# Performance work log

Hardware: AMD Instinct MI355X
Metric: run time of the kernel (lower is better)

Reference implementation:

```python
import jax, jax.numpy as jnp
import numpy as np

E, H_HEADS, WS = 512, 16, 8
HEAD_D = E // H_HEADS
LN_EPS = 1e-5


def layernorm(x, g, b):
    mu = jnp.mean(x, axis=-1, keepdims=True)
    var = jnp.mean((x - mu) ** 2, axis=-1, keepdims=True)
    return (x - mu) / jnp.sqrt(var + LN_EPS) * g + b


def setup_inputs() -> dict:
    key = jax.random.key(0)
    ks = jax.random.split(key, 10)
    s = 0.02
    return {
        "x": jax.random.normal(ks[0], (4, 4096, E), jnp.float32),
        "in_proj_w": jax.random.normal(ks[1], (3 * E, E), jnp.float32) * s,
        "in_proj_b": jnp.zeros((3 * E,), jnp.float32),
        "out_w": jax.random.normal(ks[2], (E, E), jnp.float32) * s,
        "out_b": jnp.zeros((E,), jnp.float32),
        "ln1_g": jnp.ones((E,), jnp.float32),
        "ln1_b": jnp.zeros((E,), jnp.float32),
        "w1": jax.random.normal(ks[3], (4 * E, E), jnp.float32) * s,
        "b1": jnp.zeros((4 * E,), jnp.float32),
        "w2": jax.random.normal(ks[4], (E, 4 * E), jnp.float32) * s,
        "b2": jnp.zeros((E,), jnp.float32),
        "ln2_g": jnp.ones((E,), jnp.float32),
        "ln2_b": jnp.zeros((E,), jnp.float32),
        "num_patches_h": 64,
        "num_patches_w": 64,
    }


def reference(x, in_proj_w, in_proj_b, out_w, out_b, ln1_g, ln1_b,
              w1, b1, w2, b2, ln2_g, ln2_b, num_patches_h, num_patches_w):
    B, P, _ = x.shape
    Hp, Wp = num_patches_h, num_patches_w  # 64 divisible by WS -> no padding branch
    nwh, nww = Hp // WS, Wp // WS
    # window partition: (B, Hp, Wp, E) -> (B*nW, WS*WS, E)
    xw = x.reshape(B, nwh, WS, nww, WS, E).transpose(0, 1, 3, 2, 4, 5)
    xw = xw.reshape(B * nwh * nww, WS * WS, E)
    # nn.MultiheadAttention default batch_first=False: axis0 is SEQ (L=B*nW),
    # axis1 is BATCH (N=WS*WS). Reproduce that literal semantics.
    L, N = xw.shape[0], xw.shape[1]
    qkv = xw @ in_proj_w.T + in_proj_b          # (L, N, 3E)
    q, k, v = jnp.split(qkv, 3, axis=-1)
    qh = q.reshape(L, N, H_HEADS, HEAD_D)
    kh = k.reshape(L, N, H_HEADS, HEAD_D)
    vh = v.reshape(L, N, H_HEADS, HEAD_D)
    scale = 1.0 / np.sqrt(HEAD_D)
    scores = jnp.einsum('lnhd,mnhd->nhlm', qh, kh) * scale  # (N, h, L, L)
    attn = jax.nn.softmax(scores, axis=-1)
    o = jnp.einsum('nhlm,mnhd->lnhd', attn, vh).reshape(L, N, E)
    attn_out = o @ out_w.T + out_b
    y = layernorm(xw + attn_out, ln1_g, ln1_b)
    ffn = jax.nn.gelu(y @ w1.T + b1, approximate=False) @ w2.T + b2
    y = layernorm(y + ffn, ln2_g, ln2_b)
    # window unpartition
    y = y.reshape(B, nwh, nww, WS, WS, E).transpose(0, 1, 3, 2, 4, 5)
    return y.reshape(B, Hp * Wp, E)[:, :P, :]
```

## Files before the change

### kernel.cpp

```cpp
#include <hip/hip_runtime.h>
#include <cmath>


typedef _Float16 half8 __attribute__((ext_vector_type(8)));
typedef _Float16 half4v __attribute__((ext_vector_type(4)));
typedef float f32x4 __attribute__((ext_vector_type(4)));

#define GLOBAL_AS(p) ((const __attribute__((address_space(1))) void*)(p))
#define LDS_AS(p) ((__attribute__((address_space(3))) void*)(p))

__device__ __forceinline__ void gload_lds16(const _Float16* g, _Float16* l) {
  __builtin_amdgcn_global_load_lds(GLOBAL_AS(g), LDS_AS(l), 16, 0, 0);
}

__device__ __forceinline__ float wave_sum(float v) {
#pragma unroll
  for (int off = 32; off > 0; off >>= 1) v += __shfl_xor(v, off, 64);
  return v;
}

__device__ __forceinline__ float gelu_fast(float x) {
  const float y = 1.5957691216057308f * (x + 0.044715f * x * x * x);
  const float e = __expf(y);
  const float t = 1.0f - 2.0f / (e + 1.0f);
  return 0.5f * x * (1.0f + t);
}

__global__ __launch_bounds__(256) void castw4_kernel(
    const float* __restrict__ s0, _Float16* __restrict__ d0,
    const float* __restrict__ s1, _Float16* __restrict__ d1,
    const float* __restrict__ s2, _Float16* __restrict__ d2,
    const float* __restrict__ s3, _Float16* __restrict__ d3) {
  int b = blockIdx.x;
  const float* s; _Float16* d;
  if (b < 768) { s = s0; d = d0; }
  else if (b < 1024) { s = s1; d = d1; b -= 768; }
  else if (b < 2048) { s = s2; d = d2; b -= 1024; }
  else { s = s3; d = d3; b -= 2048; }
  const int i = (b * 256 + threadIdx.x) * 4;
  const float4 v = *(const float4*)&s[i];
  half4v o;
  o[0] = (_Float16)v.x; o[1] = (_Float16)v.y; o[2] = (_Float16)v.z; o[3] = (_Float16)v.w;
  *(half4v*)&d[i] = o;
}

__global__ __launch_bounds__(256) void gather_x_kernel(const float* __restrict__ x,
                                                       _Float16* __restrict__ xw) {
  const int idx = blockIdx.x * 256 + threadIdx.x;
  const int t = idx >> 6;
  const int e0 = (idx & 63) << 3;
  const int l = t >> 6, n = t & 63;
  const int bb = l >> 6, wh = (l >> 3) & 7, ww = l & 7;
  const int pi = n >> 3, pj = n & 7;
  const int xrow = (bb * 4096 + (wh * 8 + pi) * 64 + (ww * 8 + pj)) * 512;
  const float4 a = *(const float4*)&x[xrow + e0];
  const float4 b = *(const float4*)&x[xrow + e0 + 4];
  half8 o;
  o[0] = (_Float16)a.x; o[1] = (_Float16)a.y; o[2] = (_Float16)a.z; o[3] = (_Float16)a.w;
  o[4] = (_Float16)b.x; o[5] = (_Float16)b.y; o[6] = (_Float16)b.z; o[7] = (_Float16)b.w;
  *(half8*)&xw[t * 512 + e0] = o;
}

template <int EPI, int K>
__global__ __launch_bounds__(512, 2) void gemm8_kernel(
    const _Float16* __restrict__ A, const _Float16* __restrict__ B,
    const float* __restrict__ bias, _Float16* __restrict__ C, int N) {
  constexpr int NT = K / 64;
  constexpr int TA = 256 * 64;
  constexpr int TB = 128 * 64;
  constexpr int TT = TA + TB;
  __shared__ _Float16 L[3][TT];

  const int tid = threadIdx.x, lane = tid & 63, wave = tid >> 6;
  const int wr = wave >> 1, wc = wave & 1;
  const int lr = lane & 15, g = lane >> 4;

  const int nbn = N >> 7;
  const int cpx = gridDim.x >> 3;
  const int wg = (blockIdx.x & 7) * cpx + (blockIdx.x >> 3);
  const int bm = wg / nbn, bn = wg % nbn;

  const int scol = ((lane & 7) ^ (lane >> 3)) << 3;
  const int srow = lane >> 3;
  const _Float16* aS = A + (size_t)(bm * 256 + wave * 8 + srow) * K + scol;
  const _Float16* bS = B + (size_t)(bn * 128 + wave * 8 + srow) * K + scol;

  auto stage = [&](int s, int tt, int h) {
    const int koff = tt * 64;
    _Float16* Ls = &L[s][0];
    if (h == 0) {
      gload_lds16(aS + (size_t)0 * 64 * K + koff, &Ls[(0 * 64 + wave * 8) * 64]);
      gload_lds16(aS + (size_t)1 * 64 * K + koff, &Ls[(1 * 64 + wave * 8) * 64]);
      gload_lds16(aS + (size_t)2 * 64 * K + koff, &Ls[(2 * 64 + wave * 8) * 64]);
    } else {
      gload_lds16(aS + (size_t)3 * 64 * K + koff, &Ls[(3 * 64 + wave * 8) * 64]);
      gload_lds16(bS + (size_t)0 * 64 * K + koff, &Ls[TA + (0 * 64 + wave * 8) * 64]);
      gload_lds16(bS + (size_t)1 * 64 * K + koff, &Ls[TA + (1 * 64 + wave * 8) * 64]);
    }
  };

  const int sw0 = ((g ^ (lr & 7)) << 3);
  const int sw1 = (((4 + g) ^ (lr & 7)) << 3);
  int arow[4], brow[4];
#pragma unroll
  for (int m = 0; m < 4; ++m) arow[m] = (wr * 64 + m * 16 + lr) * 64;
#pragma unroll
  for (int n = 0; n < 4; ++n) brow[n] = TA + (wc * 64 + n * 16 + lr) * 64;

  f32x4 acc[4][4] = {};

  stage(0, 0, 0); stage(0, 0, 1);
  stage(1, 1, 0); stage(1, 1, 1);
  asm volatile("s_waitcnt vmcnt(6)" ::: "memory");
  asm volatile("s_barrier" ::: "memory");

  int p = 0, s = 2;
  for (int t = 0; t < NT; ++t) {
    const _Float16* Lp = &L[p][0];
    half8 af[4], bf[4];
#pragma unroll
    for (int m = 0; m < 4; ++m) af[m] = *(const half8*)&Lp[arow[m] + sw0];
#pragma unroll
    for (int n = 0; n < 4; ++n) bf[n] = *(const half8*)&Lp[brow[n] + sw0];
    if (t + 2 < NT) stage(s, t + 2, 0);
    __builtin_amdgcn_s_setprio(1);
#pragma unroll
    for (int m = 0; m < 4; ++m)
#pragma unroll
      for (int n = 0; n < 4; ++n)
        acc[m][n] = __builtin_amdgcn_mfma_f32_16x16x32_f16(af[m], bf[n], acc[m][n], 0, 0, 0);
    __builtin_amdgcn_s_setprio(0);
#pragma unroll
    for (int m = 0; m < 4; ++m) af[m] = *(const half8*)&Lp[arow[m] + sw1];
#pragma unroll
    for (int n = 0; n < 4; ++n) bf[n] = *(const half8*)&Lp[brow[n] + sw1];
    if (t + 2 < NT) stage(s, t + 2, 1);
    __builtin_amdgcn_s_setprio(1);
#pragma unroll
    for (int m = 0; m < 4; ++m)
#pragma unroll
      for (int n = 0; n < 4; ++n)
        acc[m][n] = __builtin_amdgcn_mfma_f32_16x16x32_f16(af[m], bf[n], acc[m][n], 0, 0, 0);
    __builtin_amdgcn_s_setprio(0);
    asm volatile("s_waitcnt lgkmcnt(0)" ::: "memory");
    if (t + 2 < NT)      asm volatile("s_waitcnt vmcnt(6)" ::: "memory");
    else if (t + 1 < NT) asm volatile("s_waitcnt vmcnt(0)" ::: "memory");
    asm volatile("s_barrier" ::: "memory");
    p = (p == 2) ? 0 : p + 1;
    s = (s == 2) ? 0 : s + 1;
  }

  float bsv[4];
#pragma unroll
  for (int n = 0; n < 4; ++n) bsv[n] = bias[bn * 128 + wc * 64 + n * 16 + lr];
  _Float16* Lc = &L[0][0] + wave * 4096;
#pragma unroll
  for (int m = 0; m < 4; ++m)
#pragma unroll
    for (int n = 0; n < 4; ++n)
#pragma unroll
      for (int r = 0; r < 4; ++r) {
        float v = acc[m][n][r] + bsv[n];
        if (EPI == 1) v = gelu_fast(v);
        const int row = m * 16 + g * 4 + r;
        const int col = n * 16 + lr;
        Lc[row * 64 + (col ^ ((row & 7) << 3))] = (_Float16)v;
      }
  asm volatile("s_waitcnt lgkmcnt(0)" ::: "memory");
  const int rrow = lane >> 3, slot = lane & 7;
  const int grow = bm * 256 + wr * 64;
  const int gcol = bn * 128 + wc * 64 + slot * 8;
#pragma unroll
  for (int blk = 0; blk < 8; ++blk) {
    const int row = blk * 8 + rrow;
    const half8 vv = *(const half8*)&Lc[row * 64 + ((slot ^ (row & 7)) << 3)];
    *(half8*)&C[(size_t)(grow + row) * N + gcol] = vv;
  }
}

__global__ __launch_bounds__(256) void attn_kernel(const _Float16* __restrict__ qkv,
                                                   _Float16* __restrict__ o_out) {
  const int n = blockIdx.x & 63;
  const int h = blockIdx.x >> 6;
  __shared__ _Float16 Ksh[256 * 40];
  __shared__ _Float16 Vt[32 * 264];
  __shared__ _Float16 Pw[4 * 64 * 72];
  const int tid = threadIdx.x;
  const int wq = tid >> 6, lane = tid & 63;
  const int lr = lane & 15, g = lane >> 4;
  const int hq = h * 32;

#pragma unroll
  for (int pass = 0; pass < 4; ++pass) {
    const int e = pass * 2048 + tid * 8;
    const int m = e >> 5, d = e & 31;
    const int base = (m * 64 + n) * 1536 + hq;
    const half8 k8 = *(const half8*)&qkv[base + 512 + d];
    const half8 v8 = *(const half8*)&qkv[base + 1024 + d];
    *(half8*)&Ksh[m * 40 + d] = k8;
#pragma unroll
    for (int j = 0; j < 8; ++j) Vt[(d + j) * 264 + m] = v8[j];
  }
  half8 qf[4];
#pragma unroll
  for (int qt = 0; qt < 4; ++qt) {
    const int qg = wq * 64 + qt * 16 + lr;
    qf[qt] = *(const half8*)&qkv[(qg * 64 + n) * 1536 + hq + g * 8];
  }
  __syncthreads();

  f32x4 o[4][2] = {};
  float den[4] = {0.f, 0.f, 0.f, 0.f};
  const float scale = 0.17677669529663687f;
  _Float16* P = &Pw[wq * (64 * 72)];

  for (int it = 0; it < 4; ++it) {
    const int k0 = it * 64;
#pragma unroll
    for (int qt = 0; qt < 4; ++qt) {
#pragma unroll
      for (int kt = 0; kt < 4; ++kt) {
        const half8 kf = *(const half8*)&Ksh[(k0 + kt * 16 + lr) * 40 + g * 8];
        const f32x4 z = {0.f, 0.f, 0.f, 0.f};
        f32x4 st = __builtin_amdgcn_mfma_f32_16x16x32_f16(kf, qf[qt], z, 0, 0, 0);
        const float p0 = __expf(st[0] * scale);
        const float p1 = __expf(st[1] * scale);
        const float p2 = __expf(st[2] * scale);
        const float p3 = __expf(st[3] * scale);
        den[qt] += (p0 + p1) + (p2 + p3);
        half4v w;
        w[0] = (_Float16)p0; w[1] = (_Float16)p1;
        w[2] = (_Float16)p2; w[3] = (_Float16)p3;
        *(half4v*)&P[(qt * 16 + lr) * 72 + kt * 16 + g * 4] = w;
      }
    }
    __syncthreads();
#pragma unroll
    for (int qt = 0; qt < 4; ++qt) {
#pragma unroll
      for (int ks = 0; ks < 2; ++ks) {
        const half8 pf = *(const half8*)&P[(qt * 16 + lr) * 72 + ks * 32 + g * 8];
#pragma unroll
        for (int dt = 0; dt < 2; ++dt) {
          const half8 vf = *(const half8*)&Vt[(dt * 16 + lr) * 264 + k0 + ks * 32 + g * 8];
          o[qt][dt] = __builtin_amdgcn_mfma_f32_16x16x32_f16(pf, vf, o[qt][dt], 0, 0, 0);
        }
      }
    }
    __syncthreads();
  }

#pragma unroll
  for (int qt = 0; qt < 4; ++qt) {
    float dq = den[qt];
    dq += __shfl_xor(dq, 16);
    dq += __shfl_xor(dq, 32);
    const float inv = 1.0f / dq;
#pragma unroll
    for (int r = 0; r < 4; ++r) {
      const float invr = __shfl(inv, g * 4 + r);
      const int qg = wq * 64 + qt * 16 + g * 4 + r;
      const int obase = (qg * 64 + n) * 512 + hq;
#pragma unroll
      for (int dt = 0; dt < 2; ++dt)
        o_out[obase + dt * 16 + lr] = (_Float16)(o[qt][dt][r] * invr);
    }
  }
}

template <int FINAL>
__global__ __launch_bounds__(256) void ln_kernel(
    const float* __restrict__ res32, const _Float16* __restrict__ add16,
    const float* __restrict__ g, const float* __restrict__ b,
    float* __restrict__ out32, _Float16* __restrict__ out16) {
  const int t = blockIdx.x * 4 + (threadIdx.x >> 6);
  const int lane = threadIdx.x & 63;
  const int e0 = lane << 3;
  const int l = t >> 6, n = t & 63;
  const int bb = l >> 6, wh = (l >> 3) & 7, ww = l & 7;
  const int pi = n >> 3, pj = n & 7;
  const int xrow = (bb * 4096 + (wh * 8 + pi) * 64 + (ww * 8 + pj)) * 512;
  const int trow = t * 512;
  const int rbase = (FINAL ? trow : xrow) + e0;
  const float4 ra = *(const float4*)&res32[rbase];
  const float4 rb = *(const float4*)&res32[rbase + 4];
  const half8 a8 = *(const half8*)&add16[trow + e0];
  float v[8];
  v[0] = ra.x + (float)a8[0]; v[1] = ra.y + (float)a8[1];
  v[2] = ra.z + (float)a8[2]; v[3] = ra.w + (float)a8[3];
  v[4] = rb.x + (float)a8[4]; v[5] = rb.y + (float)a8[5];
  v[6] = rb.z + (float)a8[6]; v[7] = rb.w + (float)a8[7];
  float sm = 0.f;
#pragma unroll
  for (int e = 0; e < 8; ++e) sm += v[e];
  sm = wave_sum(sm);
  const float mu = sm * (1.0f / 512.0f);
  float vs = 0.f;
#pragma unroll
  for (int e = 0; e < 8; ++e) { const float d = v[e] - mu; vs += d * d; }
  vs = wave_sum(vs);
  const float rstd = rsqrtf(vs * (1.0f / 512.0f) + 1e-5f);
  const float4 g1 = *(const float4*)&g[e0];
  const float4 g2 = *(const float4*)&g[e0 + 4];
  const float4 b1 = *(const float4*)&b[e0];
  const float4 b2 = *(const float4*)&b[e0 + 4];
  float y[8];
  y[0] = (v[0] - mu) * rstd * g1.x + b1.x; y[1] = (v[1] - mu) * rstd * g1.y + b1.y;
  y[2] = (v[2] - mu) * rstd * g1.z + b1.z; y[3] = (v[3] - mu) * rstd * g1.w + b1.w;
  y[4] = (v[4] - mu) * rstd * g2.x + b2.x; y[5] = (v[5] - mu) * rstd * g2.y + b2.y;
  y[6] = (v[6] - mu) * rstd * g2.z + b2.z; y[7] = (v[7] - mu) * rstd * g2.w + b2.w;
  if (FINAL) {
    *(float4*)&out32[xrow + e0] = make_float4(y[0], y[1], y[2], y[3]);
    *(float4*)&out32[xrow + e0 + 4] = make_float4(y[4], y[5], y[6], y[7]);
  } else {
    *(float4*)&out32[trow + e0] = make_float4(y[0], y[1], y[2], y[3]);
    *(float4*)&out32[trow + e0 + 4] = make_float4(y[4], y[5], y[6], y[7]);
    half8 o16;
#pragma unroll
    for (int e = 0; e < 8; ++e) o16[e] = (_Float16)y[e];
    *(half8*)&out16[trow + e0] = o16;
  }
}

extern "C" void kernel_launch(void* const* d_in, const int* in_sizes, int n_in,
                              void* d_out, int out_size, void* d_ws, size_t ws_size,
                              hipStream_t stream) {
  const float* x    = (const float*)d_in[0];
  const float* ipw  = (const float*)d_in[1];
  const float* ipb  = (const float*)d_in[2];
  const float* outw = (const float*)d_in[3];
  const float* outb = (const float*)d_in[4];
  const float* ln1g = (const float*)d_in[5];
  const float* ln1b = (const float*)d_in[6];
  const float* w1   = (const float*)d_in[7];
  const float* b1   = (const float*)d_in[8];
  const float* w2   = (const float*)d_in[9];
  const float* b2   = (const float*)d_in[10];
  const float* ln2g = (const float*)d_in[11];
  const float* ln2b = (const float*)d_in[12];
  float* out = (float*)d_out;
  char* ws = (char*)d_ws;

  _Float16* wqkv_h = (_Float16*)(ws + 0);
  _Float16* wout_h = (_Float16*)(ws + 1572864);
  _Float16* w1_h   = (_Float16*)(ws + 2097152);
  _Float16* w2_h   = (_Float16*)(ws + 4194304);
  _Float16* xw_h   = (_Float16*)(ws + 6291456);
  _Float16* qkv_h  = (_Float16*)(ws + 23068672);
  _Float16* attn_h = (_Float16*)(ws + 90177536);
  _Float16* ao_h   = (_Float16*)(ws + 106954752);
  float*    y32    = (float*)(ws + 123731968);
  _Float16* h_h = qkv_h;
  _Float16* f_h = attn_h;
  _Float16* y16 = xw_h;

  castw4_kernel<<<3072, 256, 0, stream>>>(ipw, wqkv_h, outw, wout_h, w1, w1_h, w2, w2_h);
  gather_x_kernel<<<4096, 256, 0, stream>>>(x, xw_h);
  gemm8_kernel<0, 512><<<768, 512, 0, stream>>>(xw_h, wqkv_h, ipb, qkv_h, 1536);
  attn_kernel<<<1024, 256, 0, stream>>>(qkv_h, attn_h);
  gemm8_kernel<0, 512><<<256, 512, 0, stream>>>(attn_h, wout_h, outb, ao_h, 512);
  ln_kernel<0><<<4096, 256, 0, stream>>>(x, ao_h, ln1g, ln1b, y32, y16);
  gemm8_kernel<1, 512><<<1024, 512, 0, stream>>>(y16, w1_h, b1, h_h, 2048);
  gemm8_kernel<0, 2048><<<256, 512, 0, stream>>>(h_h, w2_h, b2, f_h, 512);
  ln_kernel<1><<<4096, 256, 0, stream>>>(y32, f_h, ln2g, ln2b, out, nullptr);
}
```

Baseline: 225.6 us.

## Add 256x256-tile GEMM kernel for QKV and FFN1 projections

Adds a new GEMM variant with a 256x256 output tile per workgroup, double-buffered LDS instead of triple-buffered, and 8 waves arranged 2x4 with each wave computing 128x64. It replaces the 256x128 kernel for the QKV projection and the first FFN GEMM. The larger tile raises arithmetic intensity and reuse of A and B tiles, which cuts global and LDS traffic per FLOP. In exchange each wave holds 128 accumulator values, which raises register pressure and may lower occupancy. The grids are also halved, so there are fewer workgroups to spread across the CUs.

New measurement: 251.0 us. 1.11x slower.

```diff
diff --git a/kernel.cpp b/kernel.cpp
--- a/kernel.cpp
+++ b/kernel.cpp
@@ -59,6 +59,111 @@
   o[0] = (_Float16)a.x; o[1] = (_Float16)a.y; o[2] = (_Float16)a.z; o[3] = (_Float16)a.w;
   o[4] = (_Float16)b.x; o[5] = (_Float16)b.y; o[6] = (_Float16)b.z; o[7] = (_Float16)b.w;
   *(half8*)&xw[t * 512 + e0] = o;
+}
+
+template <int EPI, int K>
+__global__ __launch_bounds__(512, 2) void gemm16_kernel(
+    const _Float16* __restrict__ A, const _Float16* __restrict__ B,
+    const float* __restrict__ bias, _Float16* __restrict__ C, int N) {
+  constexpr int NT = K / 64;
+  constexpr int TA = 256 * 64;
+  constexpr int TT = 2 * TA;
+  __shared__ _Float16 L[2][TT];
+
+  const int tid = threadIdx.x, lane = tid & 63, wave = tid >> 6;
+  const int wr = wave >> 2, wc = wave & 3;
+  const int lr = lane & 15, g = lane >> 4;
+
+  const int nbn = N >> 8;
+  const int cpx = gridDim.x >> 3;
+  const int wg = (blockIdx.x & 7) * cpx + (blockIdx.x >> 3);
+  const int bm = wg / nbn, bn = wg % nbn;
+
+  const int scol = ((lane & 7) ^ (lane >> 3)) << 3;
+  const int srow = lane >> 3;
+  const _Float16* aS = A + (size_t)(bm * 256 + wave * 8 + srow) * K + scol;
+  const _Float16* bS = B + (size_t)(bn * 256 + wave * 8 + srow) * K + scol;
+
+  auto stage = [&](int b, int tt) {
+    const int koff = tt * 64;
+    _Float16* Ls = &L[b][0];
+#pragma unroll
+    for (int i = 0; i < 4; ++i)
+      gload_lds16(aS + (size_t)(i * 64) * K + koff, &Ls[(i * 64 + wave * 8) * 64]);
+#pragma unroll
+    for (int i = 0; i < 4; ++i)
+      gload_lds16(bS + (size_t)(i * 64) * K + koff, &Ls[TA + (i * 64 + wave * 8) * 64]);
+  };
+
+  const int sw0 = ((g ^ (lr & 7)) << 3);
+  const int sw1 = (((4 + g) ^ (lr & 7)) << 3);
+  int arow[8], brow[4];
+#pragma unroll
+  for (int m = 0; m < 8; ++m) arow[m] = (wr * 128 + m * 16 + lr) * 64;
+#pragma unroll
+  for (int n = 0; n < 4; ++n) brow[n] = TA + (wc * 64 + n * 16 + lr) * 64;
+
+  f32x4 acc[8][4] = {};
+
+  stage(0, 0);
+  __syncthreads();
+
+  for (int t = 0; t < NT; ++t) {
+    const int p = t & 1;
+    const _Float16* Lp = &L[p][0];
+    if (t + 1 < NT) stage(p ^ 1, t + 1);
+    half8 af[8], bf[4];
+#pragma unroll
+    for (int m = 0; m < 8; ++m) af[m] = *(const half8*)&Lp[arow[m] + sw0];
+#pragma unroll
+    for (int n = 0; n < 4; ++n) bf[n] = *(const half8*)&Lp[brow[n] + sw0];
+    __builtin_amdgcn_s_setprio(1);
+#pragma unroll
+    for (int m = 0; m < 8; ++m)
+#pragma unroll
+      for (int n = 0; n < 4; ++n)
+        acc[m][n] = __builtin_amdgcn_mfma_f32_16x16x32_f16(af[m], bf[n], acc[m][n], 0, 0, 0);
+    __builtin_amdgcn_s_setprio(0);
+#pragma unroll
+    for (int m = 0; m < 8; ++m) af[m] = *(const half8*)&Lp[arow[m] + sw1];
+#pragma unroll
+    for (int n = 0; n < 4; ++n) bf[n] = *(const half8*)&Lp[brow[n] + sw1];
+    __builtin_amdgcn_s_setprio(1);
+#pragma unroll
+    for (int m = 0; m < 8; ++m)
+#pragma unroll
+      for (int n = 0; n < 4; ++n)
+        acc[m][n] = __builtin_amdgcn_mfma_f32_16x16x32_f16(af[m], bf[n], acc[m][n], 0, 0, 0);
+    __builtin_amdgcn_s_setprio(0);
+    __syncthreads();
+  }
+
+  float bsv[4];
+#pragma unroll
+  for (int n = 0; n < 4; ++n) bsv[n] = bias[bn * 256 + wc * 64 + n * 16 + lr];
+  _Float16* Lc = &L[0][0] + wave * 8192;
+#pragma unroll
+  for (int m = 0; m < 8; ++m)
+#pragma unroll
+    for (int n = 0; n < 4; ++n)
+#pragma unroll
+      for (int r = 0; r < 4; ++r) {
+        float v = acc[m][n][r] + bsv[n];
+        if (EPI == 1) v = gelu_fast(v);
+        const int row = m * 16 + g * 4 + r;
+        const int col = n * 16 + lr;
+        Lc[row * 64 + (col ^ ((row & 7) << 3))] = (_Float16)v;
+      }
+  asm volatile("s_waitcnt lgkmcnt(0)" ::: "memory");
+  const int rrow = lane >> 3, slot = lane & 7;
+  const int grow = bm * 256 + wr * 128;
+  const int gcol = bn * 256 + wc * 64 + slot * 8;
+#pragma unroll
+  for (int blk = 0; blk < 16; ++blk) {
+    const int row = blk * 8 + rrow;
+    const half8 vv = *(const half8*)&Lc[row * 64 + ((slot ^ (row & 7)) << 3)];
+    *(half8*)&C[(size_t)(grow + row) * N + gcol] = vv;
+  }
 }
 
 template <int EPI, int K>
@@ -356,11 +461,11 @@
 
   castw4_kernel<<<3072, 256, 0, stream>>>(ipw, wqkv_h, outw, wout_h, w1, w1_h, w2, w2_h);
   gather_x_kernel<<<4096, 256, 0, stream>>>(x, xw_h);
-  gemm8_kernel<0, 512><<<768, 512, 0, stream>>>(xw_h, wqkv_h, ipb, qkv_h, 1536);
+  gemm16_kernel<0, 512><<<384, 512, 0, stream>>>(xw_h, wqkv_h, ipb, qkv_h, 1536);
   attn_kernel<<<1024, 256, 0, stream>>>(qkv_h, attn_h);
   gemm8_kernel<0, 512><<<256, 512, 0, stream>>>(attn_h, wout_h, outb, ao_h, 512);
   ln_kernel<0><<<4096, 256, 0, stream>>>(x, ao_h, ln1g, ln1b, y32, y16);
-  gemm8_kernel<1, 512><<<1024, 512, 0, stream>>>(y16, w1_h, b1, h_h, 2048);
+  gemm16_kernel<1, 512><<<512, 512, 0, stream>>>(y16, w1_h, b1, h_h, 2048);
   gemm8_kernel<0, 2048><<<256, 512, 0, stream>>>(h_h, w2_h, b2, f_h, 512);
   ln_kernel<1><<<4096, 256, 0, stream>>>(y32, f_h, ln2g, ln2b, out, nullptr);
 }
```

## Replace triple-buffered 256x128 GEMM with single-buffer 128x128 tiles at higher occupancy

Applied to the files above, without the earlier changes.

The GEMM kernel drops from 512-thread blocks with 256x128 tiles and a three-stage LDS pipeline to 256-thread blocks with 128x128 tiles and one LDS buffer. Each iteration loads a k-slice, syncs, computes, then syncs again, so software prefetch is gone. The launch bounds now request 4 blocks per CU and grids double. Latency hiding is meant to come from more concurrent blocks rather than multi-buffering, at the cost of less A-tile reuse and exposed global-load latency on every step.

Result: faster. 208.4 us (-7.6%).

```diff
diff --git a/kernel.cpp b/kernel.cpp
--- a/kernel.cpp
+++ b/kernel.cpp
@@ -62,14 +62,12 @@
 }
 
 template <int EPI, int K>
-__global__ __launch_bounds__(512, 2) void gemm8_kernel(
+__global__ __launch_bounds__(256, 4) void gemml_kernel(
     const _Float16* __restrict__ A, const _Float16* __restrict__ B,
     const float* __restrict__ bias, _Float16* __restrict__ C, int N) {
   constexpr int NT = K / 64;
-  constexpr int TA = 256 * 64;
-  constexpr int TB = 128 * 64;
-  constexpr int TT = TA + TB;
-  __shared__ _Float16 L[3][TT];
+  constexpr int TA = 128 * 64;
+  __shared__ _Float16 L[2 * TA];
 
   const int tid = threadIdx.x, lane = tid & 63, wave = tid >> 6;
   const int wr = wave >> 1, wc = wave & 1;
@@ -82,22 +80,8 @@
 
   const int scol = ((lane & 7) ^ (lane >> 3)) << 3;
   const int srow = lane >> 3;
-  const _Float16* aS = A + (size_t)(bm * 256 + wave * 8 + srow) * K + scol;
+  const _Float16* aS = A + (size_t)(bm * 128 + wave * 8 + srow) * K + scol;
   const _Float16* bS = B + (size_t)(bn * 128 + wave * 8 + srow) * K + scol;
-
-  auto stage = [&](int s, int tt, int h) {
-    const int koff = tt * 64;
-    _Float16* Ls = &L[s][0];
-    if (h == 0) {
-      gload_lds16(aS + (size_t)0 * 64 * K + koff, &Ls[(0 * 64 + wave * 8) * 64]);
-      gload_lds16(aS + (size_t)1 * 64 * K + koff, &Ls[(1 * 64 + wave * 8) * 64]);
-      gload_lds16(aS + (size_t)2 * 64 * K + koff, &Ls[(2 * 64 + wave * 8) * 64]);
-    } else {
-      gload_lds16(aS + (size_t)3 * 64 * K + koff, &Ls[(3 * 64 + wave * 8) * 64]);
-      gload_lds16(bS + (size_t)0 * 64 * K + koff, &Ls[TA + (0 * 64 + wave * 8) * 64]);
-      gload_lds16(bS + (size_t)1 * 64 * K + koff, &Ls[TA + (1 * 64 + wave * 8) * 64]);
-    }
-  };
 
   const int sw0 = ((g ^ (lr & 7)) << 3);
   const int sw1 = (((4 + g) ^ (lr & 7)) << 3);
@@ -109,20 +93,20 @@
 
   f32x4 acc[4][4] = {};
 
-  stage(0, 0, 0); stage(0, 0, 1);
-  stage(1, 1, 0); stage(1, 1, 1);
-  asm volatile("s_waitcnt vmcnt(6)" ::: "memory");
-  asm volatile("s_barrier" ::: "memory");
-
-  int p = 0, s = 2;
   for (int t = 0; t < NT; ++t) {
-    const _Float16* Lp = &L[p][0];
+    const int koff = t * 64;
+#pragma unroll
+    for (int i = 0; i < 4; ++i)
+      gload_lds16(aS + (size_t)(i * 32) * K + koff, &L[(i * 32 + wave * 8) * 64]);
+#pragma unroll
+    for (int i = 0; i < 4; ++i)
+      gload_lds16(bS + (size_t)(i * 32) * K + koff, &L[TA + (i * 32 + wave * 8) * 64]);
+    __syncthreads();
     half8 af[4], bf[4];
 #pragma unroll
-    for (int m = 0; m < 4; ++m) af[m] = *(const half8*)&Lp[arow[m] + sw0];
-#pragma unroll
-    for (int n = 0; n < 4; ++n) bf[n] = *(const half8*)&Lp[brow[n] + sw0];
-    if (t + 2 < NT) stage(s, t + 2, 0);
+    for (int m = 0; m < 4; ++m) af[m] = *(const half8*)&L[arow[m] + sw0];
+#pragma unroll
+    for (int n = 0; n < 4; ++n) bf[n] = *(const half8*)&L[brow[n] + sw0];
     __builtin_amdgcn_s_setprio(1);
 #pragma unroll
     for (int m = 0; m < 4; ++m)
@@ -131,10 +115,9 @@
         acc[m][n] = __builtin_amdgcn_mfma_f32_16x16x32_f16(af[m], bf[n], acc[m][n], 0, 0, 0);
     __builtin_amdgcn_s_setprio(0);
 #pragma unroll
-    for (int m = 0; m < 4; ++m) af[m] = *(const half8*)&Lp[arow[m] + sw1];
-#pragma unroll
-    for (int n = 0; n < 4; ++n) bf[n] = *(const half8*)&Lp[brow[n] + sw1];
-    if (t + 2 < NT) stage(s, t + 2, 1);
+    for (int m = 0; m < 4; ++m) af[m] = *(const half8*)&L[arow[m] + sw1];
+#pragma unroll
+    for (int n = 0; n < 4; ++n) bf[n] = *(const half8*)&L[brow[n] + sw1];
     __builtin_amdgcn_s_setprio(1);
 #pragma unroll
     for (int m = 0; m < 4; ++m)
@@ -142,18 +125,13 @@
       for (int n = 0; n < 4; ++n)
         acc[m][n] = __builtin_amdgcn_mfma_f32_16x16x32_f16(af[m], bf[n], acc[m][n], 0, 0, 0);
     __builtin_amdgcn_s_setprio(0);
-    asm volatile("s_waitcnt lgkmcnt(0)" ::: "memory");
-    if (t + 2 < NT)      asm volatile("s_waitcnt vmcnt(6)" ::: "memory");
-    else if (t + 1 < NT) asm volatile("s_waitcnt vmcnt(0)" ::: "memory");
-    asm volatile("s_barrier" ::: "memory");
-    p = (p == 2) ? 0 : p + 1;
-    s = (s == 2) ? 0 : s + 1;
+    __syncthreads();
   }
 
   float bsv[4];
 #pragma unroll
   for (int n = 0; n < 4; ++n) bsv[n] = bias[bn * 128 + wc * 64 + n * 16 + lr];
-  _Float16* Lc = &L[0][0] + wave * 4096;
+  _Float16* Lc = &L[0] + wave * 4096;
 #pragma unroll
   for (int m = 0; m < 4; ++m)
 #pragma unroll
@@ -168,7 +146,7 @@
       }
   asm volatile("s_waitcnt lgkmcnt(0)" ::: "memory");
   const int rrow = lane >> 3, slot = lane & 7;
-  const int grow = bm * 256 + wr * 64;
+  const int grow = bm * 128 + wr * 64;
   const int gcol = bn * 128 + wc * 64 + slot * 8;
 #pragma unroll
   for (int blk = 0; blk < 8; ++blk) {
@@ -356,11 +334,11 @@
 
   castw4_kernel<<<3072, 256, 0, stream>>>(ipw, wqkv_h, outw, wout_h, w1, w1_h, w2, w2_h);
   gather_x_kernel<<<4096, 256, 0, stream>>>(x, xw_h);
-  gemm8_kernel<0, 512><<<768, 512, 0, stream>>>(xw_h, wqkv_h, ipb, qkv_h, 1536);
+  gemml_kernel<0, 512><<<1536, 256, 0, stream>>>(xw_h, wqkv_h, ipb, qkv_h, 1536);
   attn_kernel<<<1024, 256, 0, stream>>>(qkv_h, attn_h);
-  gemm8_kernel<0, 512><<<256, 512, 0, stream>>>(attn_h, wout_h, outb, ao_h, 512);
+  gemml_kernel<0, 512><<<512, 256, 0, stream>>>(attn_h, wout_h, outb, ao_h, 512);
   ln_kernel<0><<<4096, 256, 0, stream>>>(x, ao_h, ln1g, ln1b, y32, y16);
-  gemm8_kernel<1, 512><<<1024, 512, 0, stream>>>(y16, w1_h, b1, h_h, 2048);
-  gemm8_kernel<0, 2048><<<256, 512, 0, stream>>>(h_h, w2_h, b2, f_h, 512);
+  gemml_kernel<1, 512><<<2048, 256, 0, stream>>>(y16, w1_h, b1, h_h, 2048);
+  gemml_kernel<0, 2048><<<512, 256, 0, stream>>>(h_h, w2_h, b2, f_h, 512);
   ln_kernel<1><<<4096, 256, 0, stream>>>(y32, f_h, ln2g, ln2b, out, nullptr);
 }
```
